# Kernel optimization log

Hardware: AMD Instinct MI355X
Metric: run time of the kernel (lower is better)

## Reference

```python
import jax, jax.numpy as jnp
import numpy as np

NEG_SLOPE_GAT = 0.2   # PyG GATConv default negative_slope
NEG_SLOPE = 0.01      # torch.nn.LeakyReLU default
NUM_AISLES = 20       # aisle_nrs drawn from [0,20); matches aisle_nrs.max()+1


def leaky(x, s):
    return jnp.where(x >= 0, x, s * x)


def gat_conv(x, src, dst, W, a_src, a_dst, b, n_nodes):
    """Single-head PyG GATConv (self-loops already appended to src/dst)."""
    h = x @ W                                        # [N, C]
    es = h @ a_src                                   # [N]
    ed = h @ a_dst                                   # [N]
    e = leaky(es[src] + ed[dst], NEG_SLOPE_GAT)      # [E] per-edge score
    m = jax.ops.segment_max(e, dst, num_segments=n_nodes)
    w = jnp.exp(e - m[dst])
    z = jax.ops.segment_sum(w, dst, num_segments=n_nodes)
    alpha = w / z[dst]                               # segment softmax over incoming edges
    out = jax.ops.segment_sum(h[src] * alpha[:, None], dst, num_segments=n_nodes)
    return out + b


def setup_inputs() -> dict:
    key = jax.random.key(0)
    ks = jax.random.split(key, 32)
    B, N, E = 16, 2048, 32768
    Fin, H, O, HA = 32, 128, 64, 256

    def glorot(k, shape):
        fan = shape[0] + shape[-1]
        return jax.random.uniform(k, shape, jnp.float32, -1.0, 1.0) * np.sqrt(6.0 / fan)

    inp = {
        "graph_nodes": jax.random.normal(ks[0], (B, N, Fin), jnp.float32),
        "aisle_nrs": jax.random.randint(ks[1], (B, N), 0, NUM_AISLES),
        "graph_edge_links": jax.random.randint(ks[2], (B, 2, E), 0, N),
        "mask": jax.random.randint(ks[3], (B, N), 0, 2),
        "picks_left": jax.random.randint(ks[4], (B,), 0, 100),
        # GAT layer 1: Fin -> H
        "W1": glorot(ks[5], (Fin, H)), "as1": glorot(ks[6], (H,)), "ad1": glorot(ks[7], (H,)), "b1": jnp.zeros((H,), jnp.float32),
        # GAT layer 2: H -> H
        "W2": glorot(ks[8], (H, H)), "as2": glorot(ks[9], (H,)), "ad2": glorot(ks[10], (H,)), "b2": jnp.zeros((H,), jnp.float32),
        # GAT layer 3: H -> O
        "W3": glorot(ks[11], (H, O)), "as3": glorot(ks[12], (O,)), "ad3": glorot(ks[13], (O,)), "b3": jnp.zeros((O,), jnp.float32),
        # post-embedding MLP head
        "lw1": glorot(ks[14], (2 * O, HA)), "lb1": jnp.zeros((HA,), jnp.float32),
        "lw2": glorot(ks[15], (HA, O)), "lb2": jnp.zeros((O,), jnp.float32),
        "lw3": glorot(ks[16], (O, 1)), "lb3": jnp.zeros((1,), jnp.float32),
    }
    return inp


def reference(graph_nodes, aisle_nrs, graph_edge_links, mask, picks_left,
              W1, as1, ad1, b1, W2, as2, ad2, b2, W3, as3, ad3, b3,
              lw1, lb1, lw2, lb2, lw3, lb3):
    B, N, Fin = graph_nodes.shape
    NT = B * N
    x = graph_nodes.reshape(NT, Fin)

    # batch the graphs: offset per-graph edge indices, append self-loops
    off = (jnp.arange(B) * N)[:, None]
    src = (graph_edge_links[:, 0, :] + off).reshape(-1)
    dst = (graph_edge_links[:, 1, :] + off).reshape(-1)
    loops = jnp.arange(NT)
    src = jnp.concatenate([src, loops])
    dst = jnp.concatenate([dst, loops])

    x = gat_conv(x, src, dst, W1, as1, ad1, b1, NT)
    x = gat_conv(x, src, dst, W2, as2, ad2, b2, NT)
    x = gat_conv(x, src, dst, W3, as3, ad3, b3, NT)

    # scatter-mean aisle embedding
    batch_idx = jnp.repeat(jnp.arange(B), N)
    aid = aisle_nrs.reshape(-1) + batch_idx * NUM_AISLES   # [NT]
    S = B * NUM_AISLES
    ssum = jax.ops.segment_sum(x, aid, num_segments=S)
    cnt = jax.ops.segment_sum(jnp.ones((NT,), x.dtype), aid, num_segments=S)
    emb = ssum / jnp.maximum(cnt, 1.0)[:, None]

    x = jnp.concatenate([x, emb[aid]], axis=1)             # [NT, 2*O]
    x = leaky(x @ lw1 + lb1, NEG_SLOPE)
    x = leaky(x @ lw2 + lb2, NEG_SLOPE)
    x = (x @ lw3 + lb3).reshape(B, N)

    logits = jnp.where(mask != 0, x, -jnp.inf)
    return jax.nn.softmax(logits, axis=1)
```

## Files before the change

### kernel.cpp

```cpp
#include <hip/hip_runtime.h>
#include <hip/hip_bf16.h>
#include <math.h>

#define BATCH 16
#define NNODE 2048
#define EPG   32768
#define NT    (BATCH * NNODE)
#define ET    (BATCH * EPG + NT)
#define NUM_AISLES 20
#define SEG   (BATCH * NUM_AISLES)
#define NEG_GAT 0.2f
#define NEG_MLP 0.01f
#define ACHUNK 8
#define CAP 64

typedef __attribute__((ext_vector_type(8))) short s16x8;
typedef __attribute__((ext_vector_type(4))) float f32x4;

__device__ __forceinline__ void split_bf16(float v, unsigned short& hi, unsigned short& lo) {
    unsigned int u = __float_as_uint(v);
    unsigned int r = u + 0x7FFFu + ((u >> 16) & 1u);
    hi = (unsigned short)(r >> 16);
    float fh = __uint_as_float(((unsigned int)hi) << 16);
    float rem = v - fh;
    unsigned int u2 = __float_as_uint(rem);
    unsigned int r2 = u2 + 0x7FFFu + ((u2 >> 16) & 1u);
    lo = (unsigned short)(r2 >> 16);
}

__global__ __launch_bounds__(256) void edge_scatter(const int* __restrict__ links,
                                                    int* __restrict__ cnt,
                                                    int* __restrict__ col_bkt) {
    int b = blockIdx.x;
    int s, d;
    if (b < 2048) {
        int xcd = b & 7, idx = b >> 3;
        int g = xcd * 2 + (idx >> 7);
        int chunk = idx & 127;
        int i = chunk * 256 + threadIdx.x;
        const int* pb = links + (size_t)g * 2 * EPG;
        s = pb[i] + (g << 11);
        d = pb[EPG + i] + (g << 11);
    } else {
        int b2 = b - 2048;
        int xcd = b2 & 7, idx = b2 >> 3;
        int g = xcd * 2 + (idx >> 3);
        int chunk = idx & 7;
        s = d = g * NNODE + chunk * 256 + threadIdx.x;
    }
    int pos = atomicAdd(&cnt[d], 1);
    if (pos < CAP) col_bkt[d * CAP + pos] = s;
}

template <int K, int NOUT, int COLS, bool LEAKY, bool ATTN, bool FINAL, bool CONCAT>
__global__ __launch_bounds__(256) void gemm_mfma(const float* __restrict__ A,
                                                 const float* __restrict__ W,
                                                 const float* __restrict__ bias,
                                                 float* __restrict__ out,
                                                 const float* __restrict__ a_src,
                                                 const float* __restrict__ a_dst,
                                                 float* __restrict__ es,
                                                 float* __restrict__ ed,
                                                 const float* __restrict__ emb,
                                                 const int* __restrict__ aisle,
                                                 const float* __restrict__ lw3,
                                                 const float* __restrict__ lb3,
                                                 const int* __restrict__ mask,
                                                 float* __restrict__ logits) {
    constexpr int C = COLS / 16;
    constexpr int LDW = K + 8;

    __shared__ unsigned short Wh[COLS * LDW], Wl[COLS * LDW];

    const int tid = threadIdx.x;
    const int wave = tid >> 6, lane = tid & 63;
    const int quad = lane >> 4, l15 = lane & 15;
    const int row0 = blockIdx.x * 64;
    const int c0 = blockIdx.y * COLS;
    const int m = row0 + wave * 16 + l15;

    for (int i = tid; i < K * COLS; i += 256) {
        int k = i / COLS;
        int n = i - k * COLS;
        unsigned short h, l;
        split_bf16(W[(size_t)k * NOUT + c0 + n], h, l);
        Wh[n * LDW + k] = h;
        Wl[n * LDW + k] = l;
    }
    __syncthreads();

    f32x4 acc[C];
#pragma unroll
    for (int c = 0; c < C; ++c)
#pragma unroll
        for (int v = 0; v < 4; ++v) acc[c][v] = 0.f;

    union SU { s16x8 v; unsigned short u[8]; };

    for (int kc = 0; kc < K; kc += 32) {
        const int off = kc + quad * 8;
        const float* srcp;
        if constexpr (CONCAT) {
            if (off < 64) {
                srcp = A + (size_t)m * 64 + off;
            } else {
                int g = m >> 11;
                srcp = emb + ((size_t)(g * NUM_AISLES + aisle[m])) * 64 + (off - 64);
            }
        } else {
            srcp = A + (size_t)m * K + off;
        }
        float4 v0 = ((const float4*)srcp)[0];
        float4 v1 = ((const float4*)srcp)[1];
        float a8[8] = {v0.x, v0.y, v0.z, v0.w, v1.x, v1.y, v1.z, v1.w};
        SU ah, al;
#pragma unroll
        for (int j = 0; j < 8; ++j) split_bf16(a8[j], ah.u[j], al.u[j]);

#pragma unroll
        for (int c = 0; c < C; ++c) {
            int woff = (c * 16 + l15) * LDW + kc + quad * 8;
            s16x8 wh = *(const s16x8*)&Wh[woff];
            s16x8 wl = *(const s16x8*)&Wl[woff];
            acc[c] = __builtin_amdgcn_mfma_f32_16x16x32_bf16(ah.v, wh, acc[c], 0, 0, 0);
            acc[c] = __builtin_amdgcn_mfma_f32_16x16x32_bf16(ah.v, wl, acc[c], 0, 0, 0);
            acc[c] = __builtin_amdgcn_mfma_f32_16x16x32_bf16(al.v, wh, acc[c], 0, 0, 0);
        }
    }
    if constexpr (FINAL) {
#pragma unroll
        for (int reg = 0; reg < 4; ++reg) {
            float p = 0.f;
#pragma unroll
            for (int c = 0; c < C; ++c) {
                int colx = c * 16 + l15;
                float v = acc[c][reg] + bias[colx];
                v = v >= 0.f ? v : NEG_MLP * v;
                p += v * lw3[colx];
            }
#pragma unroll
            for (int mk = 1; mk < 16; mk <<= 1) p += __shfl_xor(p, mk, 64);
            if (l15 == 0) {
                int row = row0 + wave * 16 + quad * 4 + reg;
                float lg = p + lb3[0];
                logits[row] = (mask[row] != 0) ? lg : -INFINITY;
            }
        }
    } else {
#pragma unroll
        for (int c = 0; c < C; ++c) {
            int colx = c0 + c * 16 + l15;
            float bv = bias ? bias[colx] : 0.f;
#pragma unroll
            for (int reg = 0; reg < 4; ++reg) {
                int row = row0 + wave * 16 + quad * 4 + reg;
                float v = acc[c][reg] + bv;
                if (LEAKY) v = v >= 0.f ? v : NEG_MLP * v;
                out[(size_t)row * NOUT + colx] = v;
            }
        }
        if constexpr (ATTN) {
#pragma unroll
            for (int reg = 0; reg < 4; ++reg) {
                float ps = 0.f, pd = 0.f;
#pragma unroll
                for (int c = 0; c < C; ++c) {
                    int colx = c * 16 + l15;
                    float v = acc[c][reg];
                    ps += v * a_src[colx];
                    pd += v * a_dst[colx];
                }
#pragma unroll
                for (int mk = 1; mk < 16; mk <<= 1) {
                    ps += __shfl_xor(ps, mk, 64);
                    pd += __shfl_xor(pd, mk, 64);
                }
                if (l15 == 0) {
                    int row = row0 + wave * 16 + quad * 4 + reg;
                    es[row] = ps;
                    ed[row] = pd;
                }
            }
        }
    }
}

template <int HD>
__global__ __launch_bounds__(256) void gat_aggregate(const float* __restrict__ h,
                                                     const float* __restrict__ es,
                                                     const float* __restrict__ ed,
                                                     const int* __restrict__ cnt,
                                                     const int* __restrict__ col_bkt,
                                                     const float* __restrict__ bias,
                                                     float* __restrict__ out) {
    int b = blockIdx.x;
    int xcd = b & 7, q = b >> 3;
    int graph = xcd * 2 + (q >> 9);
    int node = graph * NNODE + (q & 511) * 4 + (threadIdx.x >> 6);
    int lane = threadIdx.x & 63;
    int deg = cnt[node];
    deg = deg < CAP ? deg : CAP;
    float edv = ed[node];

    float e0 = -INFINITY;
    int c0v = 0;
    if (lane < deg) {
        c0v = col_bkt[node * CAP + lane];
        float e = es[c0v] + edv;
        e0 = e >= 0.f ? e : NEG_GAT * e;
    }
    float m = e0;
#pragma unroll
    for (int off = 32; off; off >>= 1) m = fmaxf(m, __shfl_xor(m, off, 64));
    float z = __expf(e0 - m);
#pragma unroll
    for (int off = 32; off; off >>= 1) z += __shfl_xor(z, off, 64);
    float w0 = __expf(e0 - m) / z;

    const int quad = lane >> 4, l15 = lane & 15;
    if (HD == 128) {
        float a0 = 0.f, a1 = 0.f, a2 = 0.f, a3 = 0.f;
        float a4 = 0.f, a5 = 0.f, a6 = 0.f, a7 = 0.f;
        for (int jj = 0; jj < deg; jj += 4) {
            int j2 = jj + quad;
            int s = __shfl(c0v, j2, 64);
            float w = __shfl(w0, j2, 64);
            const float* base = h + (size_t)s * 128 + l15 * 8;
            float4 v0 = *(const float4*)base;
            float4 v1 = *(const float4*)(base + 4);
            a0 += w * v0.x; a1 += w * v0.y; a2 += w * v0.z; a3 += w * v0.w;
            a4 += w * v1.x; a5 += w * v1.y; a6 += w * v1.z; a7 += w * v1.w;
        }
#pragma unroll
        for (int off = 16; off <= 32; off <<= 1) {
            a0 += __shfl_xor(a0, off, 64); a1 += __shfl_xor(a1, off, 64);
            a2 += __shfl_xor(a2, off, 64); a3 += __shfl_xor(a3, off, 64);
            a4 += __shfl_xor(a4, off, 64); a5 += __shfl_xor(a5, off, 64);
            a6 += __shfl_xor(a6, off, 64); a7 += __shfl_xor(a7, off, 64);
        }
        if (quad == 0) {
            const float* bb = bias + l15 * 8;
            float4 o0, o1;
            o0.x = a0 + bb[0]; o0.y = a1 + bb[1]; o0.z = a2 + bb[2]; o0.w = a3 + bb[3];
            o1.x = a4 + bb[4]; o1.y = a5 + bb[5]; o1.z = a6 + bb[6]; o1.w = a7 + bb[7];
            float* op = out + (size_t)node * 128 + l15 * 8;
            *(float4*)op = o0;
            *(float4*)(op + 4) = o1;
        }
    } else {
        float a0 = 0.f, a1 = 0.f, a2 = 0.f, a3 = 0.f;
        for (int jj = 0; jj < deg; jj += 4) {
            int j2 = jj + quad;
            int s = __shfl(c0v, j2, 64);
            float w = __shfl(w0, j2, 64);
            float4 v = *(const float4*)(h + (size_t)s * 64 + l15 * 4);
            a0 += w * v.x; a1 += w * v.y; a2 += w * v.z; a3 += w * v.w;
        }
#pragma unroll
        for (int off = 16; off <= 32; off <<= 1) {
            a0 += __shfl_xor(a0, off, 64); a1 += __shfl_xor(a1, off, 64);
            a2 += __shfl_xor(a2, off, 64); a3 += __shfl_xor(a3, off, 64);
        }
        if (quad == 0) {
            const float* bb = bias + l15 * 4;
            float4 o;
            o.x = a0 + bb[0]; o.y = a1 + bb[1]; o.z = a2 + bb[2]; o.w = a3 + bb[3];
            *(float4*)(out + (size_t)node * 64 + l15 * 4) = o;
        }
    }
}

__global__ __launch_bounds__(256) void aisle_partial(const float* __restrict__ x3,
                                                     const int* __restrict__ aisle,
                                                     float* __restrict__ psum,
                                                     int* __restrict__ pcnt) {
    int g = blockIdx.x >> 3;
    int ch = blockIdx.x & 7;
    int f = threadIdx.x & 63;
    int stripe = threadIdx.x >> 6;

    __shared__ float sacc[4][NUM_AISLES][64];
    __shared__ int scnt[4][NUM_AISLES];
    for (int i = threadIdx.x; i < 4 * NUM_AISLES * 64; i += 256)
        ((float*)sacc)[i] = 0.f;
    for (int i = threadIdx.x; i < 4 * NUM_AISLES; i += 256)
        ((int*)scnt)[i] = 0;
    __syncthreads();

    const int* ai = aisle + g * NNODE;
    const float* xg = x3 + (size_t)g * NNODE * 64;
    int n0 = ch * 256 + stripe * 64;
#pragma unroll 4
    for (int i = 0; i < 64; ++i) {
        int n = n0 + i;
        int a = ai[n];
        float v = xg[(size_t)n * 64 + f];
        sacc[stripe][a][f] += v;
        if (f == 0) scnt[stripe][a]++;
    }
    __syncthreads();

    for (int i = threadIdx.x; i < NUM_AISLES * 64; i += 256) {
        int a = i >> 6, ff = i & 63;
        psum[((size_t)blockIdx.x * NUM_AISLES + a) * 64 + ff] =
            sacc[0][a][ff] + sacc[1][a][ff] + sacc[2][a][ff] + sacc[3][a][ff];
    }
    for (int i = threadIdx.x; i < NUM_AISLES; i += 256) {
        pcnt[blockIdx.x * NUM_AISLES + i] =
            scnt[0][i] + scnt[1][i] + scnt[2][i] + scnt[3][i];
    }
}

__global__ __launch_bounds__(256) void aisle_reduce(const float* __restrict__ psum,
                                                    const int* __restrict__ pcnt,
                                                    float* __restrict__ emb) {
    int idx = blockIdx.x * 256 + threadIdx.x;
    if (idx >= SEG * 64) return;
    int seg = idx >> 6;
    int f = idx & 63;
    int g = seg / NUM_AISLES;
    int a = seg - g * NUM_AISLES;
    float s = 0.f;
    int c = 0;
#pragma unroll
    for (int ch = 0; ch < ACHUNK; ++ch) {
        int blk = g * ACHUNK + ch;
        s += psum[((size_t)blk * NUM_AISLES + a) * 64 + f];
        c += pcnt[blk * NUM_AISLES + a];
    }
    emb[idx] = s / fmaxf((float)c, 1.0f);
}

__global__ __launch_bounds__(256) void softmax_kernel(const float* __restrict__ logits,
                                                      float* __restrict__ out) {
    int b = blockIdx.x;
    const float* lr = logits + b * NNODE;
    __shared__ float red[4], redz[4];
    float m = -INFINITY;
    for (int i = threadIdx.x; i < NNODE; i += 256) m = fmaxf(m, lr[i]);
#pragma unroll
    for (int off = 32; off; off >>= 1) m = fmaxf(m, __shfl_xor(m, off, 64));
    if ((threadIdx.x & 63) == 0) red[threadIdx.x >> 6] = m;
    __syncthreads();
    m = fmaxf(fmaxf(red[0], red[1]), fmaxf(red[2], red[3]));
    float z = 0.f;
    for (int i = threadIdx.x; i < NNODE; i += 256) z += __expf(lr[i] - m);
#pragma unroll
    for (int off = 32; off; off >>= 1) z += __shfl_xor(z, off, 64);
    if ((threadIdx.x & 63) == 0) redz[threadIdx.x >> 6] = z;
    __syncthreads();
    z = redz[0] + redz[1] + redz[2] + redz[3];
    float invz = 1.0f / z;
    for (int i = threadIdx.x; i < NNODE; i += 256) {
        float v = lr[i];
        out[b * NNODE + i] = (v == -INFINITY) ? 0.f : __expf(v - m) * invz;
    }
}


extern "C" void kernel_launch(void* const* d_in, const int* in_sizes, int n_in,
                              void* d_out, int out_size, void* d_ws, size_t ws_size,
                              hipStream_t stream) {
    const float* gn   = (const float*)d_in[0];
    const int* aisle  = (const int*)d_in[1];
    const int* links  = (const int*)d_in[2];
    const int* mask   = (const int*)d_in[3];
    const float* W1  = (const float*)d_in[5];
    const float* as1 = (const float*)d_in[6];
    const float* ad1 = (const float*)d_in[7];
    const float* b1  = (const float*)d_in[8];
    const float* W2  = (const float*)d_in[9];
    const float* as2 = (const float*)d_in[10];
    const float* ad2 = (const float*)d_in[11];
    const float* b2  = (const float*)d_in[12];
    const float* W3  = (const float*)d_in[13];
    const float* as3 = (const float*)d_in[14];
    const float* ad3 = (const float*)d_in[15];
    const float* b3  = (const float*)d_in[16];
    const float* lw1 = (const float*)d_in[17];
    const float* lb1 = (const float*)d_in[18];
    const float* lw2 = (const float*)d_in[19];
    const float* lb2 = (const float*)d_in[20];
    const float* lw3 = (const float*)d_in[21];
    const float* lb3 = (const float*)d_in[22];
    float* out = (float*)d_out;

    float* ws = (float*)d_ws;
    float* h      = ws;
    float* xb     = h + (size_t)NT * 128;
    float* es     = xb + (size_t)NT * 128;
    float* ed     = es + NT;
    float* emb    = ed + NT;
    float* y1     = emb + SEG * 64;
    float* y2     = y1 + (size_t)NT * 256;
    float* logits = y2 + (size_t)NT * 64;
    float* psum   = logits + NT;
    int* pcnt     = (int*)(psum + 128 * NUM_AISLES * 64);
    int* row_ptr  = pcnt + 128 * NUM_AISLES;
    int* cnt      = row_ptr + NT + 1;
    int* col_bkt  = (int*)y2;

    const int EB = (ET + 255) / 256;

    hipMemsetAsync(cnt, 0, NT * sizeof(int), stream);
    edge_scatter<<<EB, 256, 0, stream>>>(links, cnt, col_bkt);

    gemm_mfma<32, 128, 128, false, true, false, false><<<dim3(NT / 64, 1), 256, 0, stream>>>(
        gn, W1, nullptr, h, as1, ad1, es, ed, nullptr, nullptr, nullptr, nullptr, nullptr, nullptr);
    gat_aggregate<128><<<NT / 4, 256, 0, stream>>>(h, es, ed, cnt, col_bkt, b1, xb);

    gemm_mfma<128, 128, 128, false, true, false, false><<<dim3(NT / 64, 1), 256, 0, stream>>>(
        xb, W2, nullptr, h, as2, ad2, es, ed, nullptr, nullptr, nullptr, nullptr, nullptr, nullptr);
    gat_aggregate<128><<<NT / 4, 256, 0, stream>>>(h, es, ed, cnt, col_bkt, b2, xb);

    gemm_mfma<128, 64, 64, false, true, false, false><<<dim3(NT / 64, 1), 256, 0, stream>>>(
        xb, W3, nullptr, h, as3, ad3, es, ed, nullptr, nullptr, nullptr, nullptr, nullptr, nullptr);
    gat_aggregate<64><<<NT / 4, 256, 0, stream>>>(h, es, ed, cnt, col_bkt, b3, xb);

    aisle_partial<<<BATCH * ACHUNK, 256, 0, stream>>>(xb, aisle, psum, pcnt);
    aisle_reduce<<<(SEG * 64 + 255) / 256, 256, 0, stream>>>(psum, pcnt, emb);

    gemm_mfma<128, 256, 128, true, false, false, true><<<dim3(NT / 64, 2), 256, 0, stream>>>(
        xb, lw1, lb1, y1, nullptr, nullptr, nullptr, nullptr, emb, aisle, nullptr, nullptr, nullptr, nullptr);
    gemm_mfma<256, 64, 64, true, false, true, false><<<dim3(NT / 64, 1), 256, 0, stream>>>(
        y1, lw2, lb2, y2, nullptr, nullptr, nullptr, nullptr, nullptr, nullptr, lw3, lb3, mask, logits);

    softmax_kernel<<<BATCH, 256, 0, stream>>>(logits, out);
}
```

Before: 313.3 us.

## Fuse small kernels via last-block-done atomics and merge edge scatter into first GEMM

Merges edge bucketing with the first GAT linear layer into one launch, folds the aisle reduce into the aisle partial kernel, and folds the softmax into the final MLP GEMM. The folds use per-graph atomic counters so the last finishing block does the reduction. This cuts three kernel launches and their inter-kernel gaps. In exchange it adds threadfences and atomics, and it drops the XCD-aware edge ordering of the old scatter.

```diff
diff --git a/kernel.cpp b/kernel.cpp
--- a/kernel.cpp
+++ b/kernel.cpp
@@ -28,55 +28,44 @@
     lo = (unsigned short)(r2 >> 16);
 }
 
-__global__ __launch_bounds__(256) void edge_scatter(const int* __restrict__ links,
-                                                    int* __restrict__ cnt,
-                                                    int* __restrict__ col_bkt) {
-    int b = blockIdx.x;
-    int s, d;
-    if (b < 2048) {
-        int xcd = b & 7, idx = b >> 3;
-        int g = xcd * 2 + (idx >> 7);
-        int chunk = idx & 127;
-        int i = chunk * 256 + threadIdx.x;
-        const int* pb = links + (size_t)g * 2 * EPG;
-        s = pb[i] + (g << 11);
-        d = pb[EPG + i] + (g << 11);
+__device__ __forceinline__ void decode_edge(int e, const int* __restrict__ links,
+                                            int& s, int& d) {
+    if (e < BATCH * EPG) {
+        int b = e >> 15;
+        int i = e & (EPG - 1);
+        const int* pb = links + (size_t)b * 2 * EPG;
+        s = pb[i] + (b << 11);
+        d = pb[EPG + i] + (b << 11);
     } else {
-        int b2 = b - 2048;
-        int xcd = b2 & 7, idx = b2 >> 3;
-        int g = xcd * 2 + (idx >> 3);
-        int chunk = idx & 7;
-        s = d = g * NNODE + chunk * 256 + threadIdx.x;
-    }
-    int pos = atomicAdd(&cnt[d], 1);
-    if (pos < CAP) col_bkt[d * CAP + pos] = s;
+        s = d = e - BATCH * EPG;
+    }
 }
 
 template <int K, int NOUT, int COLS, bool LEAKY, bool ATTN, bool FINAL, bool CONCAT>
-__global__ __launch_bounds__(256) void gemm_mfma(const float* __restrict__ A,
-                                                 const float* __restrict__ W,
-                                                 const float* __restrict__ bias,
-                                                 float* __restrict__ out,
-                                                 const float* __restrict__ a_src,
-                                                 const float* __restrict__ a_dst,
-                                                 float* __restrict__ es,
-                                                 float* __restrict__ ed,
-                                                 const float* __restrict__ emb,
-                                                 const int* __restrict__ aisle,
-                                                 const float* __restrict__ lw3,
-                                                 const float* __restrict__ lb3,
-                                                 const int* __restrict__ mask,
-                                                 float* __restrict__ logits) {
+__device__ __forceinline__ void gemm_tile(int tile, int cy,
+                                          unsigned short* Wh, unsigned short* Wl,
+                                          const float* __restrict__ A,
+                                          const float* __restrict__ W,
+                                          const float* __restrict__ bias,
+                                          float* __restrict__ out,
+                                          const float* __restrict__ a_src,
+                                          const float* __restrict__ a_dst,
+                                          float* __restrict__ es,
+                                          float* __restrict__ ed,
+                                          const float* __restrict__ emb,
+                                          const int* __restrict__ aisle,
+                                          const float* __restrict__ lw3,
+                                          const float* __restrict__ lb3,
+                                          const int* __restrict__ mask,
+                                          float* __restrict__ logits) {
     constexpr int C = COLS / 16;
     constexpr int LDW = K + 8;
-
-    __shared__ unsigned short Wh[COLS * LDW], Wl[COLS * LDW];
 
     const int tid = threadIdx.x;
     const int wave = tid >> 6, lane = tid & 63;
     const int quad = lane >> 4, l15 = lane & 15;
-    const int row0 = blockIdx.x * 64;
-    const int c0 = blockIdx.y * COLS;
+    const int row0 = tile * 64;
+    const int c0 = cy * COLS;
     const int m = row0 + wave * 16 + l15;
 
     for (int i = tid; i < K * COLS; i += 256) {
@@ -181,6 +170,94 @@
                     ed[row] = pd;
                 }
             }
+        }
+    }
+}
+
+__global__ __launch_bounds__(256) void stage0_kernel(const float* __restrict__ gn,
+                                                     const float* __restrict__ W1,
+                                                     float* __restrict__ h,
+                                                     const float* __restrict__ as1,
+                                                     const float* __restrict__ ad1,
+                                                     float* __restrict__ es,
+                                                     float* __restrict__ ed,
+                                                     const int* __restrict__ links,
+                                                     int* __restrict__ cnt,
+                                                     int* __restrict__ col_bkt) {
+    __shared__ unsigned short Wh[128 * 40], Wl[128 * 40];
+    int b = blockIdx.x;
+    if (b < 512) {
+        gemm_tile<32, 128, 128, false, true, false, false>(
+            b, 0, Wh, Wl, gn, W1, nullptr, h, as1, ad1, es, ed,
+            nullptr, nullptr, nullptr, nullptr, nullptr, nullptr);
+    } else {
+        int e = (b - 512) * 256 + threadIdx.x;
+        int s, d;
+        decode_edge(e, links, s, d);
+        int pos = atomicAdd(&cnt[d], 1);
+        if (pos < CAP) col_bkt[d * CAP + pos] = s;
+    }
+}
+
+template <int K, int NOUT, int COLS, bool LEAKY, bool ATTN, bool CONCAT>
+__global__ __launch_bounds__(256) void gemm_kernel(const float* __restrict__ A,
+                                                   const float* __restrict__ W,
+                                                   const float* __restrict__ bias,
+                                                   float* __restrict__ out,
+                                                   const float* __restrict__ a_src,
+                                                   const float* __restrict__ a_dst,
+                                                   float* __restrict__ es,
+                                                   float* __restrict__ ed,
+                                                   const float* __restrict__ emb,
+                                                   const int* __restrict__ aisle) {
+    __shared__ unsigned short Wh[COLS * (K + 8)], Wl[COLS * (K + 8)];
+    gemm_tile<K, NOUT, COLS, LEAKY, ATTN, false, CONCAT>(
+        blockIdx.x, blockIdx.y, Wh, Wl, A, W, bias, out, a_src, a_dst, es, ed,
+        emb, aisle, nullptr, nullptr, nullptr, nullptr);
+}
+
+__global__ __launch_bounds__(256) void head2_kernel(const float* __restrict__ y1,
+                                                    const float* __restrict__ lw2,
+                                                    const float* __restrict__ lb2,
+                                                    const float* __restrict__ lw3,
+                                                    const float* __restrict__ lb3,
+                                                    const int* __restrict__ mask,
+                                                    float* __restrict__ logits,
+                                                    float* __restrict__ out,
+                                                    int* __restrict__ done2) {
+    __shared__ unsigned short Wh[64 * 264], Wl[64 * 264];
+    gemm_tile<256, 64, 64, true, false, true, false>(
+        blockIdx.x, 0, Wh, Wl, y1, lw2, lb2, nullptr, nullptr, nullptr, nullptr, nullptr,
+        nullptr, nullptr, lw3, lb3, mask, logits);
+
+    int g = blockIdx.x >> 5;
+    __shared__ int sdone;
+    __threadfence();
+    __syncthreads();
+    if (threadIdx.x == 0) sdone = atomicAdd(&done2[g], 1);
+    __syncthreads();
+    if (sdone == 31) {
+        __threadfence();
+        const float* lr = logits + g * NNODE;
+        __shared__ float red[4], redz[4];
+        float m = -INFINITY;
+        for (int i = threadIdx.x; i < NNODE; i += 256) m = fmaxf(m, lr[i]);
+#pragma unroll
+        for (int off = 32; off; off >>= 1) m = fmaxf(m, __shfl_xor(m, off, 64));
+        if ((threadIdx.x & 63) == 0) red[threadIdx.x >> 6] = m;
+        __syncthreads();
+        m = fmaxf(fmaxf(red[0], red[1]), fmaxf(red[2], red[3]));
+        float z = 0.f;
+        for (int i = threadIdx.x; i < NNODE; i += 256) z += __expf(lr[i] - m);
+#pragma unroll
+        for (int off = 32; off; off >>= 1) z += __shfl_xor(z, off, 64);
+        if ((threadIdx.x & 63) == 0) redz[threadIdx.x >> 6] = z;
+        __syncthreads();
+        z = redz[0] + redz[1] + redz[2] + redz[3];
+        float invz = 1.0f / z;
+        for (int i = threadIdx.x; i < NNODE; i += 256) {
+            float v = lr[i];
+            out[g * NNODE + i] = (v == -INFINITY) ? 0.f : __expf(v - m) * invz;
         }
     }
 }
@@ -270,10 +347,12 @@
     }
 }
 
-__global__ __launch_bounds__(256) void aisle_partial(const float* __restrict__ x3,
-                                                     const int* __restrict__ aisle,
-                                                     float* __restrict__ psum,
-                                                     int* __restrict__ pcnt) {
+__global__ __launch_bounds__(256) void aisle_fused(const float* __restrict__ x3,
+                                                   const int* __restrict__ aisle,
+                                                   float* __restrict__ psum,
+                                                   int* __restrict__ pcnt,
+                                                   float* __restrict__ emb,
+                                                   int* __restrict__ done) {
     int g = blockIdx.x >> 3;
     int ch = blockIdx.x & 7;
     int f = threadIdx.x & 63;
@@ -309,51 +388,26 @@
         pcnt[blockIdx.x * NUM_AISLES + i] =
             scnt[0][i] + scnt[1][i] + scnt[2][i] + scnt[3][i];
     }
-}
-
-__global__ __launch_bounds__(256) void aisle_reduce(const float* __restrict__ psum,
-                                                    const int* __restrict__ pcnt,
-                                                    float* __restrict__ emb) {
-    int idx = blockIdx.x * 256 + threadIdx.x;
-    if (idx >= SEG * 64) return;
-    int seg = idx >> 6;
-    int f = idx & 63;
-    int g = seg / NUM_AISLES;
-    int a = seg - g * NUM_AISLES;
-    float s = 0.f;
-    int c = 0;
-#pragma unroll
-    for (int ch = 0; ch < ACHUNK; ++ch) {
-        int blk = g * ACHUNK + ch;
-        s += psum[((size_t)blk * NUM_AISLES + a) * 64 + f];
-        c += pcnt[blk * NUM_AISLES + a];
-    }
-    emb[idx] = s / fmaxf((float)c, 1.0f);
-}
-
-__global__ __launch_bounds__(256) void softmax_kernel(const float* __restrict__ logits,
-                                                      float* __restrict__ out) {
-    int b = blockIdx.x;
-    const float* lr = logits + b * NNODE;
-    __shared__ float red[4], redz[4];
-    float m = -INFINITY;
-    for (int i = threadIdx.x; i < NNODE; i += 256) m = fmaxf(m, lr[i]);
-#pragma unroll
-    for (int off = 32; off; off >>= 1) m = fmaxf(m, __shfl_xor(m, off, 64));
-    if ((threadIdx.x & 63) == 0) red[threadIdx.x >> 6] = m;
-    __syncthreads();
-    m = fmaxf(fmaxf(red[0], red[1]), fmaxf(red[2], red[3]));
-    float z = 0.f;
-    for (int i = threadIdx.x; i < NNODE; i += 256) z += __expf(lr[i] - m);
-#pragma unroll
-    for (int off = 32; off; off >>= 1) z += __shfl_xor(z, off, 64);
-    if ((threadIdx.x & 63) == 0) redz[threadIdx.x >> 6] = z;
-    __syncthreads();
-    z = redz[0] + redz[1] + redz[2] + redz[3];
-    float invz = 1.0f / z;
-    for (int i = threadIdx.x; i < NNODE; i += 256) {
-        float v = lr[i];
-        out[b * NNODE + i] = (v == -INFINITY) ? 0.f : __expf(v - m) * invz;
+
+    __shared__ int sdone;
+    __threadfence();
+    __syncthreads();
+    if (threadIdx.x == 0) sdone = atomicAdd(&done[g], 1);
+    __syncthreads();
+    if (sdone == ACHUNK - 1) {
+        __threadfence();
+        for (int idx = threadIdx.x; idx < NUM_AISLES * 64; idx += 256) {
+            int a = idx >> 6, ff = idx & 63;
+            float s = 0.f;
+            int c = 0;
+#pragma unroll
+            for (int c2 = 0; c2 < ACHUNK; ++c2) {
+                int blk = g * ACHUNK + c2;
+                s += psum[((size_t)blk * NUM_AISLES + a) * 64 + ff];
+                c += pcnt[blk * NUM_AISLES + a];
+            }
+            emb[(g * NUM_AISLES + a) * 64 + ff] = s / fmaxf((float)c, 1.0f);
+        }
     }
 }
 
@@ -398,32 +452,27 @@
     int* pcnt     = (int*)(psum + 128 * NUM_AISLES * 64);
     int* row_ptr  = pcnt + 128 * NUM_AISLES;
     int* cnt      = row_ptr + NT + 1;
+    int* done     = cnt + NT;
+    int* done2    = done + 16;
     int* col_bkt  = (int*)y2;
 
-    const int EB = (ET + 255) / 256;
-
-    hipMemsetAsync(cnt, 0, NT * sizeof(int), stream);
-    edge_scatter<<<EB, 256, 0, stream>>>(links, cnt, col_bkt);
-
-    gemm_mfma<32, 128, 128, false, true, false, false><<<dim3(NT / 64, 1), 256, 0, stream>>>(
-        gn, W1, nullptr, h, as1, ad1, es, ed, nullptr, nullptr, nullptr, nullptr, nullptr, nullptr);
+    hipMemsetAsync(cnt, 0, (NT + 64) * sizeof(int), stream);
+
+    stage0_kernel<<<512 + ET / 256, 256, 0, stream>>>(gn, W1, h, as1, ad1, es, ed,
+                                                      links, cnt, col_bkt);
     gat_aggregate<128><<<NT / 4, 256, 0, stream>>>(h, es, ed, cnt, col_bkt, b1, xb);
 
-    gemm_mfma<128, 128, 128, false, true, false, false><<<dim3(NT / 64, 1), 256, 0, stream>>>(
-        xb, W2, nullptr, h, as2, ad2, es, ed, nullptr, nullptr, nullptr, nullptr, nullptr, nullptr);
+    gemm_kernel<128, 128, 128, false, true, false><<<dim3(NT / 64, 1), 256, 0, stream>>>(
+        xb, W2, nullptr, h, as2, ad2, es, ed, nullptr, nullptr);
     gat_aggregate<128><<<NT / 4, 256, 0, stream>>>(h, es, ed, cnt, col_bkt, b2, xb);
 
-    gemm_mfma<128, 64, 64, false, true, false, false><<<dim3(NT / 64, 1), 256, 0, stream>>>(
-        xb, W3, nullptr, h, as3, ad3, es, ed, nullptr, nullptr, nullptr, nullptr, nullptr, nullptr);
+    gemm_kernel<128, 64, 64, false, true, false><<<dim3(NT / 64, 1), 256, 0, stream>>>(
+        xb, W3, nullptr, h, as3, ad3, es, ed, nullptr, nullptr);
     gat_aggregate<64><<<NT / 4, 256, 0, stream>>>(h, es, ed, cnt, col_bkt, b3, xb);
 
-    aisle_partial<<<BATCH * ACHUNK, 256, 0, stream>>>(xb, aisle, psum, pcnt);
-    aisle_reduce<<<(SEG * 64 + 255) / 256, 256, 0, stream>>>(psum, pcnt, emb);
-
-    gemm_mfma<128, 256, 128, true, false, false, true><<<dim3(NT / 64, 2), 256, 0, stream>>>(
-        xb, lw1, lb1, y1, nullptr, nullptr, nullptr, nullptr, emb, aisle, nullptr, nullptr, nullptr, nullptr);
-    gemm_mfma<256, 64, 64, true, false, true, false><<<dim3(NT / 64, 1), 256, 0, stream>>>(
-        y1, lw2, lb2, y2, nullptr, nullptr, nullptr, nullptr, nullptr, nullptr, lw3, lb3, mask, logits);
-
-    softmax_kernel<<<BATCH, 256, 0, stream>>>(logits, out);
-}
+    aisle_fused<<<BATCH * ACHUNK, 256, 0, stream>>>(xb, aisle, psum, pcnt, emb, done);
+
+    gemm_kernel<128, 256, 128, true, false, true><<<dim3(NT / 64, 2), 256, 0, stream>>>(
+        xb, lw1, lb1, y1, nullptr, nullptr, nullptr, nullptr, emb, aisle);
+    head2_kernel<<<NT / 64, 256, 0, stream>>>(y1, lw2, lb2, lw3, lb3, mask, logits, out, done2);
+}
```

Measured after the change: 342.0 us. +9.2%, slower.
